# Optimization experiments

Hardware: AMD Instinct MI355X
Metric: run time of the kernel (lower is better)

Reference implementation:

```python
import jax, jax.numpy as jnp
import numpy as np

TOP_K = 2

def setup_inputs() -> dict:
    key = jax.random.key(0)
    k1, k2, k3, k4 = jax.random.split(key, 4)
    B, T, C = 4, 2048, 1024
    E, D_FF = 8, 1024  # d_ff = 1 * n_embd
    x = jax.random.normal(k1, (B, T, C), dtype=jnp.float32)
    router_w = jax.random.normal(k2, (E, C), dtype=jnp.float32) * 0.02
    w1 = jax.random.normal(k3, (E, C, D_FF), dtype=jnp.float32) * 0.02
    w2 = jax.random.normal(k4, (E, D_FF, C), dtype=jnp.float32) * 0.02
    return {"x": x, "router_w": router_w, "w1": w1, "w2": w2}

def reference(x, router_w, w1, w2):
    B, T, C = x.shape
    x_flat = x.reshape(-1, C)                          # [N, C]
    logits = x_flat @ router_w.T                       # [N, E]
    probs = jax.nn.softmax(logits, axis=-1)
    weights, indices = jax.lax.top_k(probs, TOP_K)     # [N, K], [N, K]
    # Dense per-expert compute (same math as gathering w1/w2 per token,
    # without duplicating weight slices per token).
    hidden = jax.nn.relu(jnp.einsum('nc,ecf->nef', x_flat, w1))  # [N, E, d_ff]
    out_all = jnp.einsum('nef,efc->nec', hidden, w2)             # [N, E, C]
    sel = jnp.take_along_axis(out_all, indices[:, :, None], axis=1)  # [N, K, C]
    out = jnp.sum(sel * weights[:, :, None], axis=1)   # [N, C]
    return out.reshape(B, T, C)
```

## Files before the change

kernel.cpp:

```cpp
#include <hip/hip_runtime.h>
#include <hip/hip_bf16.h>

#define NTOK 8192
#define CDIM 1024
#define FDIM 1024
#define NEXP 8
#define BM 128
#define BN 128
#define BK 64
#define NKT (CDIM / BK)
#define MAXT 136
#define NWG (8 * MAXT)

typedef __attribute__((ext_vector_type(8))) short short8;
typedef __attribute__((ext_vector_type(4))) float f32x4;

union Pack4 { __hip_bfloat16 h[4]; unsigned long long v; };
union U4 { unsigned long long u; unsigned short s[4]; };

typedef const unsigned int __attribute__((address_space(1)))* gas_ptr;
typedef unsigned int __attribute__((address_space(3)))* las_ptr;

__device__ __forceinline__ void gload16(const void* g, void* l) {
    __builtin_amdgcn_global_load_lds(
        (gas_ptr)(unsigned long long)g,
        (las_ptr)(unsigned int)(unsigned long long)l,
        16, 0, 0);
}

__device__ __forceinline__ float bf2f(unsigned short v) {
    unsigned int t = (unsigned int)v << 16;
    return __uint_as_float(t);
}

__global__ __launch_bounds__(256) void router_kernel(
    const float* __restrict__ x, const float* __restrict__ rw,
    __hip_bfloat16* __restrict__ xb,
    int* __restrict__ cnt, int* __restrict__ rows, float* __restrict__ wts)
{
    __shared__ int lcnt[NEXP];
    __shared__ int lt[NEXP][32];
    __shared__ float lw[NEXP][32];
    __shared__ int base[NEXP];
    const int tid = threadIdx.x;
    const int wv = tid >> 6, lane = tid & 63;
    if (tid < NEXP) lcnt[tid] = 0;
    __syncthreads();

    for (int tt = 0; tt < 4; tt++) {
        const int n = blockIdx.x * 16 + wv * 4 + tt;
        float acc[NEXP];
#pragma unroll
        for (int e = 0; e < NEXP; e++) acc[e] = 0.f;
#pragma unroll
        for (int c0 = 0; c0 < CDIM; c0 += 256) {
            const size_t o = (size_t)n * CDIM + c0 + lane * 4;
            float4 xv = *(const float4*)(x + o);
            Pack4 p4;
            p4.h[0] = __float2bfloat16(xv.x); p4.h[1] = __float2bfloat16(xv.y);
            p4.h[2] = __float2bfloat16(xv.z); p4.h[3] = __float2bfloat16(xv.w);
            *(unsigned long long*)(xb + o) = p4.v;
#pragma unroll
            for (int e = 0; e < NEXP; e++) {
                float4 w4 = *(const float4*)&rw[e * CDIM + c0 + lane * 4];
                acc[e] += xv.x * w4.x + xv.y * w4.y + xv.z * w4.z + xv.w * w4.w;
            }
        }
#pragma unroll
        for (int e = 0; e < NEXP; e++) {
#pragma unroll
            for (int s = 32; s > 0; s >>= 1) acc[e] += __shfl_xor(acc[e], s);
        }
        if (lane == 0) {
            float mx = acc[0];
#pragma unroll
            for (int e = 1; e < NEXP; e++) mx = fmaxf(mx, acc[e]);
            float p[NEXP], se = 0.f;
#pragma unroll
            for (int e = 0; e < NEXP; e++) { p[e] = __expf(acc[e] - mx); se += p[e]; }
            float inv = 1.f / se;
            int i0 = 0;
#pragma unroll
            for (int e = 1; e < NEXP; e++) if (p[e] > p[i0]) i0 = e;
            int i1 = (i0 == 0) ? 1 : 0;
#pragma unroll
            for (int e = 0; e < NEXP; e++) if (e != i0 && p[e] > p[i1]) i1 = e;
            int p0 = atomicAdd(&lcnt[i0], 1);
            lt[i0][p0] = n;
            lw[i0][p0] = p[i0] * inv;
            int p1 = atomicAdd(&lcnt[i1], 1);
            lt[i1][p1] = n | (1 << 16);
            lw[i1][p1] = p[i1] * inv;
        }
    }
    __syncthreads();
    if (tid < NEXP) base[tid] = atomicAdd(&cnt[tid * 16], lcnt[tid]);
    __syncthreads();
#pragma unroll
    for (int e = 0; e < NEXP; e++) {
        for (int i = tid; i < lcnt[e]; i += 256) {
            rows[e * NTOK + base[e] + i] = lt[e][i];
            wts [e * NTOK + base[e] + i] = lw[e][i];
        }
    }
}

__global__ void scan_offsets(const int* __restrict__ cnt, int* __restrict__ offs,
                             int* __restrict__ wl)
{
    if (threadIdx.x == 0) {
        int s = 0, t = 0;
        for (int e = 0; e < NEXP; e++) {
            int me = cnt[e * 16];
            offs[e] = s; s += me;
            for (int m0 = 0; m0 < me; m0 += BM) {
                wl[1 + 2 * t] = e; wl[2 + 2 * t] = m0; t++;
            }
        }
        wl[0] = t;
    }
}

__global__ __launch_bounds__(256) void build_slots(
    const int* __restrict__ cnt, const int* __restrict__ offs,
    const int* __restrict__ rows, int* __restrict__ slot)
{
    const int e = blockIdx.y;
    const int i = blockIdx.x * 256 + threadIdx.x;
    if (i < cnt[e * 16]) {
        int p = rows[e * NTOK + i];
        slot[2 * (p & 0xFFFF) + (p >> 16)] = offs[e] + i;
    }
}

__global__ __launch_bounds__(256) void transpose_conv(
    const float* __restrict__ src, __hip_bfloat16* __restrict__ dst)
{
    __shared__ float t[64][65];
    const int e = blockIdx.z;
    const int r0 = blockIdx.x * 64, c0 = blockIdx.y * 64;
    const int tid = threadIdx.x;
    const int rr = tid >> 4;
    const int cc = (tid & 15) * 4;
#pragma unroll
    for (int j = 0; j < 4; j++) {
        int row = j * 16 + rr;
        float4 v = *(const float4*)(src + ((size_t)e * 1024 + r0 + row) * 1024 + c0 + cc);
        t[row][cc] = v.x; t[row][cc + 1] = v.y; t[row][cc + 2] = v.z; t[row][cc + 3] = v.w;
    }
    __syncthreads();
#pragma unroll
    for (int j = 0; j < 4; j++) {
        int trow = j * 16 + rr;
        Pack4 o;
#pragma unroll
        for (int k = 0; k < 4; k++) o.h[k] = __float2bfloat16(t[cc + k][trow]);
        *(unsigned long long*)(dst + ((size_t)e * 1024 + c0 + trow) * 1024 + r0 + cc) = o.v;
    }
}

__global__ __launch_bounds__(256, 2) void moe_gemm1(
    const __hip_bfloat16* __restrict__ xb, const __hip_bfloat16* __restrict__ w1t,
    const int* __restrict__ cnt, const int* __restrict__ offs,
    const int* __restrict__ wl, const int* __restrict__ rows,
    __hip_bfloat16* __restrict__ hid)
{
    const int bid = blockIdx.x;
    const int wid = (bid & 7) * MAXT + (bid >> 3);
    const int t = wid >> 3;
    if (t >= wl[0]) return;
    const int n0 = (wid & 7) * BN;
    const int e = wl[1 + 2 * t], m0 = wl[2 + 2 * t];
    const int me = cnt[e * 16], off = offs[e];
    const int tid = threadIdx.x;
    const int lane = tid & 63, wv = tid >> 6;
    const int wr = wv >> 1, wc = wv & 1;
    const int fr = lane & 15, fq = lane >> 4;
    const int fx = fr & 7;

    __shared__ alignas(16) __hip_bfloat16 smem[2][2][BM * BK];

    const int swz8 = (((lane & 7) ^ (lane >> 3))) * 8;
    const __hip_bfloat16* asrc[4];
    const __hip_bfloat16* bsrc[4];
#pragma unroll
    for (int i = 0; i < 4; i++) {
        int row = i * 32 + wv * 8 + (lane >> 3);
        int gi = m0 + row;
        int ri = gi < me ? gi : me - 1;
        int tok = rows[e * NTOK + ri] & 0xFFFF;
        asrc[i] = xb + (size_t)tok * CDIM + swz8;
        bsrc[i] = w1t + ((size_t)e * FDIM + n0 + row) * CDIM + swz8;
    }

    f32x4 acc[4][4] = {};

#pragma unroll
    for (int i = 0; i < 4; i++) {
        gload16(asrc[i], &smem[0][0][(i * 256 + wv * 64) * 8]);
        gload16(bsrc[i], &smem[0][1][(i * 256 + wv * 64) * 8]);
    }
    asm volatile("s_waitcnt lgkmcnt(0)" ::: "memory");

    int cur = 0;
    for (int kt = 0; kt < NKT; kt++) {
        __builtin_amdgcn_s_barrier();
        if (kt + 1 < NKT) {
            const int k1 = (kt + 1) * BK;
#pragma unroll
            for (int i = 0; i < 4; i++) {
                gload16(asrc[i] + k1, &smem[cur ^ 1][0][(i * 256 + wv * 64) * 8]);
                gload16(bsrc[i] + k1, &smem[cur ^ 1][1][(i * 256 + wv * 64) * 8]);
            }
            asm volatile("s_waitcnt vmcnt(8)" ::: "memory");
        } else {
            asm volatile("s_waitcnt vmcnt(0)" ::: "memory");
        }
        __builtin_amdgcn_s_barrier();
        __builtin_amdgcn_sched_barrier(0);
#pragma unroll
        for (int ks = 0; ks < 2; ks++) {
            short8 af[4], bfv[4];
#pragma unroll
            for (int m = 0; m < 4; m++)
                af[m] = *(const short8*)&smem[cur][0][
                    (wr * 64 + m * 16 + fr) * BK + (((ks * 4 + fq) ^ fx) * 8)];
#pragma unroll
            for (int n = 0; n < 4; n++)
                bfv[n] = *(const short8*)&smem[cur][1][
                    (wc * 64 + n * 16 + fr) * BK + (((ks * 4 + fq) ^ fx) * 8)];
#pragma unroll
            for (int m = 0; m < 4; m++)
#pragma unroll
                for (int n = 0; n < 4; n++)
                    acc[m][n] = __builtin_amdgcn_mfma_f32_16x16x32_bf16(
                        af[m], bfv[n], acc[m][n], 0, 0, 0);
        }
        cur ^= 1;
    }
    __syncthreads();

    __hip_bfloat16 (*Cl)[BN] = reinterpret_cast<__hip_bfloat16(*)[BN]>(&smem[0][0][0]);
#pragma unroll
    for (int m = 0; m < 4; m++)
#pragma unroll
        for (int n = 0; n < 4; n++)
#pragma unroll
            for (int r = 0; r < 4; r++) {
                int il = wr * 64 + m * 16 + fq * 4 + r;
                float v = acc[m][n][r];
                Cl[il][wc * 64 + n * 16 + fr] = __float2bfloat16(v > 0.f ? v : 0.f);
            }
    __syncthreads();
#pragma unroll
    for (int i = 0; i < 8; i++) {
        int chunk = i * 256 + tid;
        int row = chunk >> 4, c8 = (chunk & 15) * 8;
        int gi = m0 + row;
        if (gi < me)
            *(short8*)(hid + (size_t)(off + gi) * FDIM + n0 + c8) =
                *(const short8*)&Cl[row][c8];
    }
}

__global__ __launch_bounds__(256, 2) void moe_gemm2(
    const __hip_bfloat16* __restrict__ hid, const __hip_bfloat16* __restrict__ w2t,
    const int* __restrict__ cnt, const int* __restrict__ offs,
    const int* __restrict__ wl, const int* __restrict__ rows,
    const float* __restrict__ wts, __hip_bfloat16* __restrict__ ybuf,
    float* __restrict__ out)
{
    const int bid = blockIdx.x;
    const int wid = (bid & 7) * MAXT + (bid >> 3);
    const int t = wid >> 3;
    if (t >= wl[0]) return;
    const int n0 = (wid & 7) * BN;
    const int e = wl[1 + 2 * t], m0 = wl[2 + 2 * t];
    const int me = cnt[e * 16], off = offs[e];
    const int tid = threadIdx.x;
    const int lane = tid & 63, wv = tid >> 6;
    const int wr = wv >> 1, wc = wv & 1;
    const int fr = lane & 15, fq = lane >> 4;
    const int fx = fr & 7;

    __shared__ alignas(16) __hip_bfloat16 smem[2][2][BM * BK];
    __shared__ int rtok[BM];
    __shared__ float rwt[BM];

    if (tid < BM) {
        int gi = m0 + tid;
        int ri = gi < me ? gi : me - 1;
        rtok[tid] = rows[e * NTOK + ri] & 0xFFFF;
        rwt[tid] = gi < me ? wts[e * NTOK + ri] : 0.f;
    }

    const int swz8 = (((lane & 7) ^ (lane >> 3))) * 8;
    const __hip_bfloat16* asrc[4];
    const __hip_bfloat16* bsrc[4];
#pragma unroll
    for (int i = 0; i < 4; i++) {
        int row = i * 32 + wv * 8 + (lane >> 3);
        int gi = m0 + row;
        int ri = gi < me ? gi : me - 1;
        asrc[i] = hid + (size_t)(off + ri) * FDIM + swz8;
        bsrc[i] = w2t + ((size_t)e * CDIM + n0 + row) * FDIM + swz8;
    }

    f32x4 acc[4][4] = {};

#pragma unroll
    for (int i = 0; i < 4; i++) {
        gload16(asrc[i], &smem[0][0][(i * 256 + wv * 64) * 8]);
        gload16(bsrc[i], &smem[0][1][(i * 256 + wv * 64) * 8]);
    }
    asm volatile("s_waitcnt lgkmcnt(0)" ::: "memory");

    int cur = 0;
    for (int kt = 0; kt < NKT; kt++) {
        __builtin_amdgcn_s_barrier();
        if (kt + 1 < NKT) {
            const int k1 = (kt + 1) * BK;
#pragma unroll
            for (int i = 0; i < 4; i++) {
                gload16(asrc[i] + k1, &smem[cur ^ 1][0][(i * 256 + wv * 64) * 8]);
                gload16(bsrc[i] + k1, &smem[cur ^ 1][1][(i * 256 + wv * 64) * 8]);
            }
            asm volatile("s_waitcnt vmcnt(8)" ::: "memory");
        } else {
            asm volatile("s_waitcnt vmcnt(0)" ::: "memory");
        }
        __builtin_amdgcn_s_barrier();
        __builtin_amdgcn_sched_barrier(0);
#pragma unroll
        for (int ks = 0; ks < 2; ks++) {
            short8 af[4], bfv[4];
#pragma unroll
            for (int m = 0; m < 4; m++)
                af[m] = *(const short8*)&smem[cur][0][
                    (wr * 64 + m * 16 + fr) * BK + (((ks * 4 + fq) ^ fx) * 8)];
#pragma unroll
            for (int n = 0; n < 4; n++)
                bfv[n] = *(const short8*)&smem[cur][1][
                    (wc * 64 + n * 16 + fr) * BK + (((ks * 4 + fq) ^ fx) * 8)];
#pragma unroll
            for (int m = 0; m < 4; m++)
#pragma unroll
                for (int n = 0; n < 4; n++)
                    acc[m][n] = __builtin_amdgcn_mfma_f32_16x16x32_bf16(
                        af[m], bfv[n], acc[m][n], 0, 0, 0);
        }
        cur ^= 1;
    }
    __syncthreads();

    if (ybuf) {
        __hip_bfloat16 (*Cl)[BN] = reinterpret_cast<__hip_bfloat16(*)[BN]>(&smem[0][0][0]);
#pragma unroll
        for (int m = 0; m < 4; m++)
#pragma unroll
            for (int n = 0; n < 4; n++)
#pragma unroll
                for (int r = 0; r < 4; r++) {
                    int il = wr * 64 + m * 16 + fq * 4 + r;
                    Cl[il][wc * 64 + n * 16 + fr] =
                        __float2bfloat16(rwt[il] * acc[m][n][r]);
                }
        __syncthreads();
#pragma unroll
        for (int i = 0; i < 8; i++) {
            int chunk = i * 256 + tid;
            int row = chunk >> 4, c8 = (chunk & 15) * 8;
            int gi = m0 + row;
            if (gi < me)
                *(short8*)(ybuf + (size_t)(off + gi) * CDIM + n0 + c8) =
                    *(const short8*)&Cl[row][c8];
        }
    } else {
#pragma unroll
        for (int m = 0; m < 4; m++)
#pragma unroll
            for (int n = 0; n < 4; n++)
#pragma unroll
                for (int r = 0; r < 4; r++) {
                    int il = wr * 64 + m * 16 + fq * 4 + r;
                    int gi = m0 + il;
                    if (gi < me)
                        atomicAdd(&out[(size_t)rtok[il] * CDIM + n0 + wc * 64 + n * 16 + fr],
                                  rwt[il] * acc[m][n][r]);
                }
    }
}

__global__ __launch_bounds__(256) void gather_out(
    const __hip_bfloat16* __restrict__ yb, const int* __restrict__ slot,
    float* __restrict__ out)
{
    for (int n = blockIdx.x; n < NTOK; n += gridDim.x) {
        const int s0 = slot[2 * n], s1 = slot[2 * n + 1];
        const int c = threadIdx.x * 4;
        U4 a, b;
        a.u = *(const unsigned long long*)(yb + (size_t)s0 * CDIM + c);
        b.u = *(const unsigned long long*)(yb + (size_t)s1 * CDIM + c);
        float4 o;
        o.x = bf2f(a.s[0]) + bf2f(b.s[0]);
        o.y = bf2f(a.s[1]) + bf2f(b.s[1]);
        o.z = bf2f(a.s[2]) + bf2f(b.s[2]);
        o.w = bf2f(a.s[3]) + bf2f(b.s[3]);
        *(float4*)(out + (size_t)n * CDIM + c) = o;
    }
}

extern "C" void kernel_launch(void* const* d_in, const int* in_sizes, int n_in,
                              void* d_out, int out_size, void* d_ws, size_t ws_size,
                              hipStream_t stream)
{
    const float* x  = (const float*)d_in[0];
    const float* rw = (const float*)d_in[1];
    const float* w1 = (const float*)d_in[2];
    const float* w2 = (const float*)d_in[3];
    float* out = (float*)d_out;
    char* ws = (char*)d_ws;

    int* cnt  = (int*)ws;
    int* offs = (int*)(ws + 1024);
    int* wl   = (int*)(ws + 2048);
    int* rows = (int*)(ws + 4096);
    float* wts = (float*)(ws + 4096 + NEXP * NTOK * 4);
    int* slot = (int*)(ws + 4096 + 2 * NEXP * NTOK * 4);
    __hip_bfloat16* xb  = (__hip_bfloat16*)(ws + (1u << 20));
    __hip_bfloat16* w1t = (__hip_bfloat16*)(ws + (17u << 20));
    __hip_bfloat16* hid = (__hip_bfloat16*)(ws + (33u << 20));
    __hip_bfloat16* w2t = w1t;
    const bool big = ws_size >= ((size_t)98 << 20);
    __hip_bfloat16* ybuf = big ? (__hip_bfloat16*)(ws + (65u << 20)) : nullptr;

    hipMemsetAsync(cnt, 0, 1024, stream);
    if (!big)
        hipMemsetAsync(d_out, 0, (size_t)out_size * sizeof(float), stream);

    router_kernel<<<NTOK / 16, 256, 0, stream>>>(x, rw, xb, cnt, rows, wts);
    scan_offsets<<<1, 64, 0, stream>>>(cnt, offs, wl);
    build_slots<<<dim3(NTOK / 256, NEXP), 256, 0, stream>>>(cnt, offs, rows, slot);
    transpose_conv<<<dim3(16, 16, NEXP), 256, 0, stream>>>(w1, w1t);
    moe_gemm1<<<NWG, 256, 0, stream>>>(xb, w1t, cnt, offs, wl, rows, hid);
    transpose_conv<<<dim3(16, 16, NEXP), 256, 0, stream>>>(w2, w2t);
    moe_gemm2<<<NWG, 256, 0, stream>>>(hid, w2t, cnt, offs, wl, rows, wts, ybuf, out);
    if (big)
        gather_out<<<2048, 256, 0, stream>>>(ybuf, slot, out);
}
```

Measured before the change: 160.8 us.

## Enlarge MoE GEMM tiles to 256x256 with 512-thread blocks

Both expert GEMM kernels move from 128x128 tiles with 256 threads to 256x256 tiles with 512 threads. Each of the 8 waves now computes 128x64 of output, and the work-list mapping and grid size are reworked to match. The goal is more data reuse per LDS load and less global traffic on the weight and activation operands. The change also adds s_setprio around the MFMA blocks and drops a redundant lgkmcnt wait. The risks are lower occupancy (one 8-wave block per CU, LDS nearly full) and coarser tiles that can balance poorly across CUs, with a tail of only slightly more blocks than CUs.

```diff
diff --git a/kernel.cpp b/kernel.cpp
--- a/kernel.cpp
+++ b/kernel.cpp
@@ -5,12 +5,13 @@
 #define CDIM 1024
 #define FDIM 1024
 #define NEXP 8
-#define BM 128
-#define BN 128
+#define BM 256
+#define BN 256
 #define BK 64
 #define NKT (CDIM / BK)
-#define MAXT 136
-#define NWG (8 * MAXT)
+#define MAXT 72
+#define NWG (MAXT * 4)
+#define CPX (NWG / 8)
 
 typedef __attribute__((ext_vector_type(8))) short short8;
 typedef __attribute__((ext_vector_type(4))) float f32x4;
@@ -159,33 +160,34 @@
     }
 }
 
-__global__ __launch_bounds__(256, 2) void moe_gemm1(
+
+__global__ __launch_bounds__(512, 1) void moe_gemm1(
     const __hip_bfloat16* __restrict__ xb, const __hip_bfloat16* __restrict__ w1t,
     const int* __restrict__ cnt, const int* __restrict__ offs,
     const int* __restrict__ wl, const int* __restrict__ rows,
     __hip_bfloat16* __restrict__ hid)
 {
     const int bid = blockIdx.x;
-    const int wid = (bid & 7) * MAXT + (bid >> 3);
-    const int t = wid >> 3;
+    const int wid = (bid & 7) * CPX + (bid >> 3);
+    const int t = wid >> 2;
     if (t >= wl[0]) return;
-    const int n0 = (wid & 7) * BN;
+    const int n0 = (wid & 3) * BN;
     const int e = wl[1 + 2 * t], m0 = wl[2 + 2 * t];
     const int me = cnt[e * 16], off = offs[e];
     const int tid = threadIdx.x;
     const int lane = tid & 63, wv = tid >> 6;
-    const int wr = wv >> 1, wc = wv & 1;
+    const int wr = wv >> 2, wc = wv & 3;
     const int fr = lane & 15, fq = lane >> 4;
     const int fx = fr & 7;
 
     __shared__ alignas(16) __hip_bfloat16 smem[2][2][BM * BK];
 
-    const int swz8 = (((lane & 7) ^ (lane >> 3))) * 8;
+    const int swz8 = (((tid & 7) ^ ((tid >> 3) & 7))) * 8;
     const __hip_bfloat16* asrc[4];
     const __hip_bfloat16* bsrc[4];
 #pragma unroll
     for (int i = 0; i < 4; i++) {
-        int row = i * 32 + wv * 8 + (lane >> 3);
+        int row = i * 64 + (tid >> 3);
         int gi = m0 + row;
         int ri = gi < me ? gi : me - 1;
         int tok = rows[e * NTOK + ri] & 0xFFFF;
@@ -193,14 +195,13 @@
         bsrc[i] = w1t + ((size_t)e * FDIM + n0 + row) * CDIM + swz8;
     }
 
-    f32x4 acc[4][4] = {};
+    f32x4 acc[8][4] = {};
 
 #pragma unroll
     for (int i = 0; i < 4; i++) {
-        gload16(asrc[i], &smem[0][0][(i * 256 + wv * 64) * 8]);
-        gload16(bsrc[i], &smem[0][1][(i * 256 + wv * 64) * 8]);
-    }
-    asm volatile("s_waitcnt lgkmcnt(0)" ::: "memory");
+        gload16(asrc[i], &smem[0][0][(i * 512 + wv * 64) * 8]);
+        gload16(bsrc[i], &smem[0][1][(i * 512 + wv * 64) * 8]);
+    }
 
     int cur = 0;
     for (int kt = 0; kt < NKT; kt++) {
@@ -209,8 +210,8 @@
             const int k1 = (kt + 1) * BK;
 #pragma unroll
             for (int i = 0; i < 4; i++) {
-                gload16(asrc[i] + k1, &smem[cur ^ 1][0][(i * 256 + wv * 64) * 8]);
-                gload16(bsrc[i] + k1, &smem[cur ^ 1][1][(i * 256 + wv * 64) * 8]);
+                gload16(asrc[i] + k1, &smem[cur ^ 1][0][(i * 512 + wv * 64) * 8]);
+                gload16(bsrc[i] + k1, &smem[cur ^ 1][1][(i * 512 + wv * 64) * 8]);
             }
             asm volatile("s_waitcnt vmcnt(8)" ::: "memory");
         } else {
@@ -220,21 +221,22 @@
         __builtin_amdgcn_sched_barrier(0);
 #pragma unroll
         for (int ks = 0; ks < 2; ks++) {
-            short8 af[4], bfv[4];
-#pragma unroll
-            for (int m = 0; m < 4; m++)
-                af[m] = *(const short8*)&smem[cur][0][
-                    (wr * 64 + m * 16 + fr) * BK + (((ks * 4 + fq) ^ fx) * 8)];
+            short8 af[8], bfv[4];
+            const int cswz = ((ks * 4 + fq) ^ fx) * 8;
+#pragma unroll
+            for (int m = 0; m < 8; m++)
+                af[m] = *(const short8*)&smem[cur][0][(wr * 128 + m * 16 + fr) * BK + cswz];
 #pragma unroll
             for (int n = 0; n < 4; n++)
-                bfv[n] = *(const short8*)&smem[cur][1][
-                    (wc * 64 + n * 16 + fr) * BK + (((ks * 4 + fq) ^ fx) * 8)];
-#pragma unroll
-            for (int m = 0; m < 4; m++)
+                bfv[n] = *(const short8*)&smem[cur][1][(wc * 64 + n * 16 + fr) * BK + cswz];
+            __builtin_amdgcn_s_setprio(1);
+#pragma unroll
+            for (int m = 0; m < 8; m++)
 #pragma unroll
                 for (int n = 0; n < 4; n++)
                     acc[m][n] = __builtin_amdgcn_mfma_f32_16x16x32_bf16(
                         af[m], bfv[n], acc[m][n], 0, 0, 0);
+            __builtin_amdgcn_s_setprio(0);
         }
         cur ^= 1;
     }
@@ -242,20 +244,20 @@
 
     __hip_bfloat16 (*Cl)[BN] = reinterpret_cast<__hip_bfloat16(*)[BN]>(&smem[0][0][0]);
 #pragma unroll
-    for (int m = 0; m < 4; m++)
+    for (int m = 0; m < 8; m++)
 #pragma unroll
         for (int n = 0; n < 4; n++)
 #pragma unroll
             for (int r = 0; r < 4; r++) {
-                int il = wr * 64 + m * 16 + fq * 4 + r;
+                int il = wr * 128 + m * 16 + fq * 4 + r;
                 float v = acc[m][n][r];
                 Cl[il][wc * 64 + n * 16 + fr] = __float2bfloat16(v > 0.f ? v : 0.f);
             }
     __syncthreads();
 #pragma unroll
-    for (int i = 0; i < 8; i++) {
-        int chunk = i * 256 + tid;
-        int row = chunk >> 4, c8 = (chunk & 15) * 8;
+    for (int i = 0; i < 16; i++) {
+        int chunk = i * 512 + tid;
+        int row = chunk >> 5, c8 = (chunk & 31) * 8;
         int gi = m0 + row;
         if (gi < me)
             *(short8*)(hid + (size_t)(off + gi) * FDIM + n0 + c8) =
@@ -263,7 +265,7 @@
     }
 }
 
-__global__ __launch_bounds__(256, 2) void moe_gemm2(
+__global__ __launch_bounds__(512, 1) void moe_gemm2(
     const __hip_bfloat16* __restrict__ hid, const __hip_bfloat16* __restrict__ w2t,
     const int* __restrict__ cnt, const int* __restrict__ offs,
     const int* __restrict__ wl, const int* __restrict__ rows,
@@ -271,15 +273,15 @@
     float* __restrict__ out)
 {
     const int bid = blockIdx.x;
-    const int wid = (bid & 7) * MAXT + (bid >> 3);
-    const int t = wid >> 3;
+    const int wid = (bid & 7) * CPX + (bid >> 3);
+    const int t = wid >> 2;
     if (t >= wl[0]) return;
-    const int n0 = (wid & 7) * BN;
+    const int n0 = (wid & 3) * BN;
     const int e = wl[1 + 2 * t], m0 = wl[2 + 2 * t];
     const int me = cnt[e * 16], off = offs[e];
     const int tid = threadIdx.x;
     const int lane = tid & 63, wv = tid >> 6;
-    const int wr = wv >> 1, wc = wv & 1;
+    const int wr = wv >> 2, wc = wv & 3;
     const int fr = lane & 15, fq = lane >> 4;
     const int fx = fr & 7;
 
@@ -294,26 +296,25 @@
         rwt[tid] = gi < me ? wts[e * NTOK + ri] : 0.f;
     }
 
-    const int swz8 = (((lane & 7) ^ (lane >> 3))) * 8;
+    const int swz8 = (((tid & 7) ^ ((tid >> 3) & 7))) * 8;
     const __hip_bfloat16* asrc[4];
     const __hip_bfloat16* bsrc[4];
 #pragma unroll
     for (int i = 0; i < 4; i++) {
-        int row = i * 32 + wv * 8 + (lane >> 3);
+        int row = i * 64 + (tid >> 3);
         int gi = m0 + row;
         int ri = gi < me ? gi : me - 1;
         asrc[i] = hid + (size_t)(off + ri) * FDIM + swz8;
         bsrc[i] = w2t + ((size_t)e * CDIM + n0 + row) * FDIM + swz8;
     }
 
-    f32x4 acc[4][4] = {};
+    f32x4 acc[8][4] = {};
 
 #pragma unroll
     for (int i = 0; i < 4; i++) {
-        gload16(asrc[i], &smem[0][0][(i * 256 + wv * 64) * 8]);
-        gload16(bsrc[i], &smem[0][1][(i * 256 + wv * 64) * 8]);
-    }
-    asm volatile("s_waitcnt lgkmcnt(0)" ::: "memory");
+        gload16(asrc[i], &smem[0][0][(i * 512 + wv * 64) * 8]);
+        gload16(bsrc[i], &smem[0][1][(i * 512 + wv * 64) * 8]);
+    }
 
     int cur = 0;
     for (int kt = 0; kt < NKT; kt++) {
@@ -322,8 +323,8 @@
             const int k1 = (kt + 1) * BK;
 #pragma unroll
             for (int i = 0; i < 4; i++) {
-                gload16(asrc[i] + k1, &smem[cur ^ 1][0][(i * 256 + wv * 64) * 8]);
-                gload16(bsrc[i] + k1, &smem[cur ^ 1][1][(i * 256 + wv * 64) * 8]);
+                gload16(asrc[i] + k1, &smem[cur ^ 1][0][(i * 512 + wv * 64) * 8]);
+                gload16(bsrc[i] + k1, &smem[cur ^ 1][1][(i * 512 + wv * 64) * 8]);
             }
             asm volatile("s_waitcnt vmcnt(8)" ::: "memory");
         } else {
@@ -333,21 +334,22 @@
         __builtin_amdgcn_sched_barrier(0);
 #pragma unroll
         for (int ks = 0; ks < 2; ks++) {
-            short8 af[4], bfv[4];
-#pragma unroll
-            for (int m = 0; m < 4; m++)
-                af[m] = *(const short8*)&smem[cur][0][
-                    (wr * 64 + m * 16 + fr) * BK + (((ks * 4 + fq) ^ fx) * 8)];
+            short8 af[8], bfv[4];
+            const int cswz = ((ks * 4 + fq) ^ fx) * 8;
+#pragma unroll
+            for (int m = 0; m < 8; m++)
+                af[m] = *(const short8*)&smem[cur][0][(wr * 128 + m * 16 + fr) * BK + cswz];
 #pragma unroll
             for (int n = 0; n < 4; n++)
-                bfv[n] = *(const short8*)&smem[cur][1][
-                    (wc * 64 + n * 16 + fr) * BK + (((ks * 4 + fq) ^ fx) * 8)];
-#pragma unroll
-            for (int m = 0; m < 4; m++)
+                bfv[n] = *(const short8*)&smem[cur][1][(wc * 64 + n * 16 + fr) * BK + cswz];
+            __builtin_amdgcn_s_setprio(1);
+#pragma unroll
+            for (int m = 0; m < 8; m++)
 #pragma unroll
                 for (int n = 0; n < 4; n++)
                     acc[m][n] = __builtin_amdgcn_mfma_f32_16x16x32_bf16(
                         af[m], bfv[n], acc[m][n], 0, 0, 0);
+            __builtin_amdgcn_s_setprio(0);
         }
         cur ^= 1;
     }
@@ -356,20 +358,20 @@
     if (ybuf) {
         __hip_bfloat16 (*Cl)[BN] = reinterpret_cast<__hip_bfloat16(*)[BN]>(&smem[0][0][0]);
 #pragma unroll
-        for (int m = 0; m < 4; m++)
+        for (int m = 0; m < 8; m++)
 #pragma unroll
             for (int n = 0; n < 4; n++)
 #pragma unroll
                 for (int r = 0; r < 4; r++) {
-                    int il = wr * 64 + m * 16 + fq * 4 + r;
+                    int il = wr * 128 + m * 16 + fq * 4 + r;
                     Cl[il][wc * 64 + n * 16 + fr] =
                         __float2bfloat16(rwt[il] * acc[m][n][r]);
                 }
         __syncthreads();
 #pragma unroll
-        for (int i = 0; i < 8; i++) {
-            int chunk = i * 256 + tid;
-            int row = chunk >> 4, c8 = (chunk & 15) * 8;
+        for (int i = 0; i < 16; i++) {
+            int chunk = i * 512 + tid;
+            int row = chunk >> 5, c8 = (chunk & 31) * 8;
             int gi = m0 + row;
             if (gi < me)
                 *(short8*)(ybuf + (size_t)(off + gi) * CDIM + n0 + c8) =
@@ -377,12 +379,12 @@
         }
     } else {
 #pragma unroll
-        for (int m = 0; m < 4; m++)
+        for (int m = 0; m < 8; m++)
 #pragma unroll
             for (int n = 0; n < 4; n++)
 #pragma unroll
                 for (int r = 0; r < 4; r++) {
-                    int il = wr * 64 + m * 16 + fq * 4 + r;
+                    int il = wr * 128 + m * 16 + fq * 4 + r;
                     int gi = m0 + il;
                     if (gi < me)
                         atomicAdd(&out[(size_t)rtok[il] * CDIM + n0 + wc * 64 + n * 16 + fr],
@@ -442,9 +444,9 @@
     scan_offsets<<<1, 64, 0, stream>>>(cnt, offs, wl);
     build_slots<<<dim3(NTOK / 256, NEXP), 256, 0, stream>>>(cnt, offs, rows, slot);
     transpose_conv<<<dim3(16, 16, NEXP), 256, 0, stream>>>(w1, w1t);
-    moe_gemm1<<<NWG, 256, 0, stream>>>(xb, w1t, cnt, offs, wl, rows, hid);
+    moe_gemm1<<<NWG, 512, 0, stream>>>(xb, w1t, cnt, offs, wl, rows, hid);
     transpose_conv<<<dim3(16, 16, NEXP), 256, 0, stream>>>(w2, w2t);
-    moe_gemm2<<<NWG, 256, 0, stream>>>(hid, w2t, cnt, offs, wl, rows, wts, ybuf, out);
+    moe_gemm2<<<NWG, 512, 0, stream>>>(hid, w2t, cnt, offs, wl, rows, wts, ybuf, out);
     if (big)
         gather_out<<<2048, 256, 0, stream>>>(ybuf, slot, out);
 }
```

New measurement: 194.2 us. 20.7% more time.
